# Performance work log

Hardware: AMD Instinct MI355X
Metric: run time of the kernel (lower is better)

Reference implementation:

```python
import jax, jax.numpy as jnp
from jax import lax
import numpy as np

B, N_WAY, K_SHOT, Q, IMG = 8, 5, 1, 15, 84
D = 3      # repnet spatial output for imgsz=84
CF = 64    # repnet channels
C2 = CF + 2

def _conv(x, w, b):
    y = lax.conv_general_dilated(x, w, (1, 1), 'VALID', dimension_numbers=('NCHW', 'OIHW', 'NCHW'))
    return y + b[None, :, None, None]

def _maxpool2(x):
    return lax.reduce_window(x, -jnp.inf, lax.max, (1, 1, 2, 2), (1, 1, 2, 2), 'VALID')

def _avgpool5(x):
    return lax.reduce_window(x, 0.0, lax.add, (1, 1, 5, 5), (1, 1, 5, 5), 'VALID') / 25.0

def _bn(x, g, b):
    # train-mode BatchNorm2d: batch statistics over (N, H, W), biased variance, eps=1e-5
    m = jnp.mean(x, (0, 2, 3), keepdims=True)
    v = jnp.var(x, (0, 2, 3), keepdims=True)
    return (x - m) * lax.rsqrt(v + 1e-5) * g[None, :, None, None] + b[None, :, None, None]

def _repnet(x, cw1, cb1, bg1, bb1, cw2, cb2, bg2, bb2, cw3, cb3, bg3, bb3, cw4, cb4, bg4, bb4):
    x = jax.nn.relu(_bn(_maxpool2(_conv(x, cw1, cb1)), bg1, bb1))
    x = jax.nn.relu(_bn(_maxpool2(_conv(x, cw2, cb2)), bg2, bb2))
    x = jax.nn.relu(_bn(_conv(x, cw3, cb3), bg3, bb3))
    x = jax.nn.relu(_bn(_conv(x, cw4, cb4), bg4, bb4))
    return _avgpool5(x)

def _forward(support_x, support_y, query_x, query_y, cw1, cb1, bg1, bb1, cw2, cb2, bg2, bb2, cw3, cb3, bg3, bb3, cw4, cb4, bg4, bb4, gW1, gb1, gW2, gb2, gW3, gb3, gW4, gb4, fW1, fb1, fW2, fb2, fW3, fb3, fW4, fb4):
    b, setsz = support_x.shape[:2]
    q = query_x.shape[1]
    rep = lambda z: _repnet(z, cw1, cb1, bg1, bb1, cw2, cb2, bg2, bb2, cw3, cb3, bg3, bb3, cw4, cb4, bg4, bb4)
    sup = rep(support_x.reshape(b * setsz, 3, IMG, IMG)).reshape(b, setsz, CF, D, D)
    qry = rep(query_x.reshape(b * q, 3, IMG, IMG)).reshape(b, q, CF, D, D)
    sup = sup.reshape(b, N_WAY, K_SHOT, CF, D, D).sum(2)  # sum over shots -> (b, n_way, c, d, d)
    setsz = N_WAY
    sy = support_y[:, ::K_SHOT]
    ii, jj = jnp.meshgrid(jnp.arange(D), jnp.arange(D), indexing='ij')
    coord = jnp.stack([ii, jj]).astype(jnp.float32) / D  # (2, d, d): ch0 = i/d, ch1 = j/d
    sup = jnp.concatenate([sup, jnp.broadcast_to(coord, (b, setsz, 2, D, D))], axis=2)  # (b,s,66,d,d)
    qry = jnp.concatenate([qry, jnp.broadcast_to(coord, (b, q, 2, D, D))], axis=2)      # (b,q,66,d,d)
    d2 = D * D
    sup = sup.reshape(b, setsz, C2, d2)
    qry = qry.reshape(b, q, C2, d2)
    # pair feature is cat([support_feat, query_feat]); split g's first layer so the
    # (b,q,s,d2,d2,2c) pair tensor is never materialized: g1([s;q]) = s@Ws + q@Wq + b1
    Ws, Wq = gW1[:C2], gW1[C2:]
    A = jnp.einsum('bscp,ck->bspk', sup, Ws)   # (b, s, d2, 256)
    Bq = jnp.einsum('bqcp,ck->bqpk', qry, Wq)  # (b, q, d2, 256)
    h = jax.nn.relu(A[:, None, :, :, None, :] + Bq[:, :, None, None, :, :] + gb1)  # (b,q,s,d2,d2,256)
    h = jax.nn.relu(h @ gW2 + gb2)
    h = jax.nn.relu(h @ gW3 + gb3)
    h = jax.nn.relu(h @ gW4 + gb4)
    x_f = h.sum((3, 4))  # sum over all d2*d2 pixel pairs -> (b, q, s, 256)
    h = jax.nn.relu(x_f @ fW1 + fb1)
    h = jax.nn.relu(h @ fW2 + fb2)  # nn.Dropout treated as identity (deterministic reference)
    h = jax.nn.relu(h @ fW3 + fb3)
    o = h @ fW4 + fb4  # (b, q, s, 64)
    score = jnp.sqrt(jnp.sum(o * o, axis=-1))  # L2 norm over feature dim -> (b, q, s)
    n = jnp.sqrt(jnp.sum(score * score, axis=2, keepdims=True))
    score = score / n * (n * n / (1.0 + n * n))  # squash
    ap = sy[:, None, :] == query_y[:, :, None]  # exactly one True per (b, q)
    an = ~ap
    score_ap = jnp.sum(jnp.where(ap, score, 0.0), axis=2, keepdims=True)
    MARGIN = 0.2
    loss = jnp.sum(jax.nn.relu(score - score_ap + MARGIN) * an)
    return loss

def setup_inputs() -> dict:
    key = jax.random.key(0)
    ks = iter(jax.random.split(key, 48))
    nrm = lambda shape, s: jax.random.normal(next(ks), shape, jnp.float32) * s
    inp = {}
    inp['support_x'] = nrm((B, N_WAY * K_SHOT, 3, IMG, IMG), 1.0)
    inp['support_y'] = jnp.tile(jnp.arange(N_WAY, dtype=jnp.int32), (B, 1))
    inp['query_x'] = nrm((B, Q, 3, IMG, IMG), 1.0)
    inp['query_y'] = jax.random.randint(next(ks), (B, Q), 0, N_WAY, dtype=jnp.int32)
    inp['cw1'] = nrm((64, 3, 3, 3), 0.19); inp['cb1'] = nrm((64,), 0.02)
    inp['bg1'] = 1.0 + nrm((64,), 0.05); inp['bb1'] = nrm((64,), 0.02)
    inp['cw2'] = nrm((64, 64, 3, 3), 0.042); inp['cb2'] = nrm((64,), 0.02)
    inp['bg2'] = 1.0 + nrm((64,), 0.05); inp['bb2'] = nrm((64,), 0.02)
    inp['cw3'] = nrm((64, 64, 3, 3), 0.042); inp['cb3'] = nrm((64,), 0.02)
    inp['bg3'] = 1.0 + nrm((64,), 0.05); inp['bb3'] = nrm((64,), 0.02)
    inp['cw4'] = nrm((64, 64, 3, 3), 0.042); inp['cb4'] = nrm((64,), 0.02)
    inp['bg4'] = 1.0 + nrm((64,), 0.05); inp['bb4'] = nrm((64,), 0.02)
    inp['gW1'] = nrm((2 * C2, 256), 0.087); inp['gb1'] = nrm((256,), 0.02)
    inp['gW2'] = nrm((256, 256), 0.0625); inp['gb2'] = nrm((256,), 0.02)
    inp['gW3'] = nrm((256, 256), 0.0625); inp['gb3'] = nrm((256,), 0.02)
    inp['gW4'] = nrm((256, 256), 0.0625); inp['gb4'] = nrm((256,), 0.02)
    inp['fW1'] = nrm((256, 256), 0.0625); inp['fb1'] = nrm((256,), 0.02)
    inp['fW2'] = nrm((256, 256), 0.0625); inp['fb2'] = nrm((256,), 0.02)
    inp['fW3'] = nrm((256, 128), 0.0625); inp['fb3'] = nrm((128,), 0.02)
    inp['fW4'] = nrm((128, 64), 0.088); inp['fb4'] = nrm((64,), 0.02)
    return inp

def reference(support_x, support_y, query_x, query_y, cw1, cb1, bg1, bb1, cw2, cb2, bg2, bb2, cw3, cb3, bg3, bb3, cw4, cb4, bg4, bb4, gW1, gb1, gW2, gb2, gW3, gb3, gW4, gb4, fW1, fb1, fW2, fb2, fW3, fb3, fW4, fb4):
    return _forward(support_x, support_y, query_x, query_y, cw1, cb1, bg1, bb1, cw2, cb2, bg2, bb2, cw3, cb3, bg3, bb3, cw4, cb4, bg4, bb4, gW1, gb1, gW2, gb2, gW3, gb3, gW4, gb4, fW1, fb1, fW2, fb2, fW3, fb3, fW4, fb4)
```

## Files before the change

### kernel.cpp

```cpp
#include <hip/hip_runtime.h>
#include <hip/hip_bf16.h>

typedef __hip_bfloat16 bf16;
typedef __attribute__((ext_vector_type(8))) short short8;
typedef __attribute__((ext_vector_type(4))) short bfx4;
typedef __attribute__((ext_vector_type(4))) float f32x4;

#define DEV __device__ __forceinline__

static constexpr int NSUP = 40;
static constexpr int NQRY = 120;
static constexpr int NIMG = 160;
static constexpr int GM   = 48600;
static constexpr int GMP  = 48640;
static constexpr int NBS  = 128;
static constexpr int NBQ  = 384;

DEV float b2f(short s) {
    union { unsigned int u; float f; } v; v.u = ((unsigned int)(unsigned short)s) << 16; return v.f;
}
DEV short bfbits(float v) {
    bf16 h = __float2bfloat16(v);
    union { bf16 b; short s; } u; u.b = h; return u.s;
}

DEV int xcd_swz(int b, int nwg) {
    int q = nwg >> 3, r = nwg & 7;
    int x = b & 7, i = b >> 3;
    return (x < r) ? x * (q + 1) + i : r * (q + 1) + (x - r) * q + i;
}

#define GLL(gp, lp) __builtin_amdgcn_global_load_lds( \
    (const __attribute__((address_space(1))) void*)(gp), \
    (__attribute__((address_space(3))) void*)(lp), 16, 0, 0)

__global__ void nhwc4_kernel(const float* sx, const float* qx, bf16* img) {
    int idx = blockIdx.x * 256 + threadIdx.x;
    if (idx >= NIMG * 7056) return;
    int n = idx / 7056, p = idx % 7056;
    const float* im = ((n < NSUP) ? sx + (size_t)n * 3 * 7056 : qx + (size_t)(n - NSUP) * 3 * 7056) + p;
    bfx4 o;
    o[0] = bfbits(im[0]);
    o[1] = bfbits(im[7056]);
    o[2] = bfbits(im[14112]);
    o[3] = 0;
    *(bfx4*)&img[(size_t)idx * 4] = o;
}

__global__ void prep_kernel(const float* cw1, const float* cw2, const float* cw3,
                            const float* cw4, const float* gW2, const float* gW3,
                            const float* gW4, const float* fW1, const float* fW2,
                            const float* fW3, const float* fW4, const float* fb4,
                            bf16* Wc1, bf16* Wp, bf16* WTg, bf16* fWT, float* fb4p) {
    int idx = blockIdx.x * 256 + threadIdx.x;
    if (idx < 4096) {
        int oc = idx >> 6, k = idx & 63;
        int ky = k >> 4, r = k & 15;
        float v = 0.f;
        if (ky < 3 && r < 12) {
            int kx = r >> 2, ic = r & 3;
            if (ic < 3) v = cw1[oc * 27 + ic * 9 + ky * 3 + kx];
        }
        Wc1[idx] = __float2bfloat16(v);
        return;
    }
    idx -= 4096;
    if (idx < 3 * 64 * 584) {
        int L = idx / (64 * 584), r = idx % (64 * 584);
        int oc = r / 584, kk = r % 584;
        const float* src = (L == 0) ? cw2 : (L == 1) ? cw3 : cw4;
        float v = 0.f;
        if (kk < 576) {
            int ic = kk & 63, tap = kk >> 6;
            v = src[oc * 576 + ic * 9 + tap];
        }
        Wp[idx] = __float2bfloat16(v);
        return;
    }
    idx -= 3 * 64 * 584;
    if (idx < 3 * 65536) {
        int L = idx >> 16, r = idx & 65535, n = r >> 8, k = r & 255;
        const float* W = (L == 0) ? gW2 : (L == 1) ? gW3 : gW4;
        WTg[idx] = __float2bfloat16(W[k * 256 + n]);
        return;
    }
    idx -= 3 * 65536;
    if (idx < 65536) {
        int n = idx >> 8, k = idx & 255;
        fWT[idx] = __float2bfloat16(fW1[k * 256 + n]);
    } else if (idx < 131072) {
        int r = idx - 65536, n = r >> 8, k = r & 255;
        fWT[idx] = __float2bfloat16(fW2[k * 256 + n]);
    } else if (idx < 163840) {
        int r = idx - 131072, n = r >> 8, k = r & 255;
        fWT[idx] = __float2bfloat16(fW3[k * 128 + n]);
    } else if (idx < 180224) {
        int r = idx - 163840, n = r >> 7, k = r & 127;
        float v = (n < 64) ? fW4[k * 64 + n] : 0.f;
        fWT[idx] = __float2bfloat16(v);
    } else if (idx < 180352) {
        int i = idx - 180224;
        fb4p[i] = (i < 64) ? fb4[i] : 0.f;
    }
}

__global__ __launch_bounds__(256) void conv1m_kernel(
        const bf16* __restrict__ img, const bf16* __restrict__ Wc1,
        const float* __restrict__ cb1, bf16* __restrict__ out) {
    int wid = xcd_swz(blockIdx.x, NIMG * 27);
    int n = wid / 27, chunk = wid % 27;
    int wv = threadIdx.x >> 6, ln = threadIdx.x & 63;
    int pr = ln & 15, kg = ln >> 4;
    int t0 = (chunk * 4 + wv) * 16;
    int t = t0 + pr;
    int tc = t < 1681 ? t : 1680;
    int pyt = tc / 41, pxt = tc % 41;
    const bf16* ib = img + (size_t)n * 28224;

    short8 wf[4][2];
    #pragma unroll
    for (int mt = 0; mt < 4; ++mt)
        #pragma unroll
        for (int h = 0; h < 2; ++h)
            wf[mt][h] = *(const short8*)&Wc1[(size_t)(mt * 16 + pr) * 64 + h * 32 + kg * 8];

    int r8 = (kg & 1) * 8;
    int kyb = kg >> 1;
    short8 pf[4][2];
    #pragma unroll
    for (int nt = 0; nt < 4; ++nt) {
        int py = 2 * pyt + (nt >> 1), px = 2 * pxt + (nt & 1);
        #pragma unroll
        for (int h = 0; h < 2; ++h) {
            int ky = h * 2 + kyb;
            short8 f = {0, 0, 0, 0, 0, 0, 0, 0};
            if (ky < 3) {
                const bf16* p = ib + ((py + ky) * 84 + px) * 4 + r8;
                if (r8 == 0) {
                    bfx4 a0 = *(const bfx4*)p, a1 = *(const bfx4*)(p + 4);
                    f[0] = a0[0]; f[1] = a0[1]; f[2] = a0[2]; f[3] = a0[3];
                    f[4] = a1[0]; f[5] = a1[1]; f[6] = a1[2]; f[7] = a1[3];
                } else {
                    bfx4 a0 = *(const bfx4*)p;
                    f[0] = a0[0]; f[1] = a0[1]; f[2] = a0[2]; f[3] = a0[3];
                }
            }
            pf[nt][h] = f;
        }
    }

    f32x4 acc[4][4];
    #pragma unroll
    for (int a = 0; a < 4; ++a)
        #pragma unroll
        for (int b = 0; b < 4; ++b)
            #pragma unroll
            for (int r = 0; r < 4; ++r) acc[a][b][r] = 0.f;

    #pragma unroll
    for (int h = 0; h < 2; ++h)
        #pragma unroll
        for (int mt = 0; mt < 4; ++mt)
            #pragma unroll
            for (int nt = 0; nt < 4; ++nt)
                acc[mt][nt] = __builtin_amdgcn_mfma_f32_16x16x32_bf16(
                    wf[mt][h], pf[nt][h], acc[mt][nt], 0, 0, 0);

    if (t < 1681) {
        bf16* ob = out + ((size_t)n * 1681 + t) * 64;
        #pragma unroll
        for (int mt = 0; mt < 4; ++mt) {
            f32x4 v = acc[mt][0];
            #pragma unroll
            for (int nt = 1; nt < 4; ++nt)
                #pragma unroll
                for (int r = 0; r < 4; ++r) v[r] = fmaxf(v[r], acc[mt][nt][r]);
            bfx4 o;
            #pragma unroll
            for (int r = 0; r < 4; ++r) o[r] = bfbits(v[r] + cb1[mt * 16 + kg * 4 + r]);
            *(bfx4*)&ob[mt * 16 + kg * 4] = o;
        }
    }
}

__global__ void stats_nhwc_kernel(const bf16* buf, int HW, float* partial) {
    int blk = blockIdx.x;
    bool qg = blk >= NBS;
    int b0 = qg ? blk - NBS : blk;
    int nb = qg ? NBQ : NBS;
    const bf16* base = buf + (qg ? (size_t)NSUP * HW * 64 : 0);
    long rows = (long)(qg ? NQRY : NSUP) * HW;
    int tid = threadIdx.x;
    int sub = tid & 7, rl = tid >> 3;
    float s1[8], s2[8];
    #pragma unroll
    for (int j = 0; j < 8; ++j) { s1[j] = 0.f; s2[j] = 0.f; }
    for (long r = (long)b0 * 32 + rl; r < rows; r += (long)nb * 32) {
        short8 v = *(const short8*)&base[r * 64 + sub * 8];
        #pragma unroll
        for (int j = 0; j < 8; ++j) { float f = b2f(v[j]); s1[j] += f; s2[j] += f * f; }
    }
    __shared__ float l1[256][8], l2[256][8];
    #pragma unroll
    for (int j = 0; j < 8; ++j) { l1[tid][j] = s1[j]; l2[tid][j] = s2[j]; }
    __syncthreads();
    if (tid < 64) {
        int su = tid >> 3, j = tid & 7;
        float a = 0.f, b = 0.f;
        for (int k = 0; k < 32; ++k) { a += l1[su + k * 8][j]; b += l2[su + k * 8][j]; }
        partial[blk * 128 + tid] = a;
        partial[blk * 128 + 64 + tid] = b;
    }
}

__global__ __launch_bounds__(1024) void bnfin_kernel(
        const float* partial, const float* gam, const float* bet,
        int HW, float* scsh) {
    int tid = threadIdx.x;
    int out = tid >> 3;
    int part = tid & 7;
    int g = out >> 6, c = out & 63;
    int b0 = g ? NBS : 0, nb = g ? NBQ : NBS;
    float s1 = 0.f, s2 = 0.f;
    for (int b = b0 + part; b < b0 + nb; b += 8) {
        s1 += partial[b * 128 + c];
        s2 += partial[b * 128 + 64 + c];
    }
    __shared__ float r1[1024], r2[1024];
    r1[tid] = s1; r2[tid] = s2;
    __syncthreads();
    if (part == 0) {
        #pragma unroll
        for (int j = 1; j < 8; ++j) { s1 += r1[tid + j]; s2 += r2[tid + j]; }
        float cnt = (float)((g ? NQRY : NSUP)) * (float)HW;
        float mean = s1 / cnt;
        float var = s2 / cnt - mean * mean;
        float istd = rsqrtf(var + 1e-5f);
        float sc = gam[c] * istd;
        scsh[out] = sc;
        scsh[128 + out] = bet[c] - mean * sc;
    }
}

__global__ void bnrelu_nhwc_kernel(bf16* buf, const float* scsh, int HW, int total8) {
    int idx = blockIdx.x * 256 + threadIdx.x;
    if (idx >= total8) return;
    size_t e0 = (size_t)idx * 8;
    int c0 = (int)(e0 & 63);
    int g = (int)(e0 / ((size_t)HW * 64)) >= NSUP ? 1 : 0;
    short8 v = *(short8*)&buf[e0];
    short8 o;
    #pragma unroll
    for (int j = 0; j < 8; ++j) {
        int c = c0 + j;
        float f = b2f(v[j]) * scsh[g * 64 + c] + scsh[128 + g * 64 + c];
        o[j] = bfbits(fmaxf(f, 0.f));
    }
    *(short8*)&buf[e0] = o;
}

template <int IW, int OW, bool POOL, int NT>
__global__ __launch_bounds__(256) void convmfma_kernel(
        const bf16* __restrict__ in, const bf16* __restrict__ Wp,
        const float* __restrict__ cb, bf16* __restrict__ out, int nwg) {
    constexpr int M  = OW * OW;
    constexpr int PW = OW / 2;
    constexpr int MP = POOL ? PW * PW : M;
    constexpr int T  = NIMG * MP;
    constexpr int NPF = POOL ? 4 : NT;

    int wid = xcd_swz(blockIdx.x, nwg);
    int wv = threadIdx.x >> 6, ln = threadIdx.x & 63;
    int pr = ln & 15, kg = ln >> 4;

    const bf16* pptr[NPF];
    int pxv[NPF];
    if (POOL) {
        int gp = (wid * 4 + wv) * 16 + pr;
        int gpc = gp < T ? gp : T - 1;
        pxv[0] = gp;
        int n = gpc / MP, pp = gpc % MP;
        int py = pp / PW, px = pp % PW;
        const bf16* ib = in + (size_t)n * (IW * IW * 64) + kg * 8;
        #pragma unroll
        for (int nt = 0; nt < 4; ++nt)
            pptr[nt] = ib + ((2 * py + (nt >> 1)) * IW + 2 * px + (nt & 1)) * 64;
    } else {
        #pragma unroll
        for (int nt = 0; nt < NT; ++nt) {
            int gp = (wid * 4 + wv) * (16 * NT) + nt * 16 + pr;
            int gpc = gp < T ? gp : T - 1;
            pxv[nt] = gp;
            int n = gpc / M, pix = gpc % M;
            int y = pix / OW, x = pix % OW;
            pptr[nt] = in + ((size_t)n * (IW * IW) + y * IW + x) * 64 + kg * 8;
        }
    }
    const bf16* wb = Wp + kg * 8;

    f32x4 acc[4][NPF];
    #pragma unroll
    for (int a = 0; a < 4; ++a)
        #pragma unroll
        for (int b = 0; b < NPF; ++b)
            #pragma unroll
            for (int r = 0; r < 4; ++r) acc[a][b][r] = 0.f;

    short8 pf_c[NPF];
    #pragma unroll
    for (int nt = 0; nt < NPF; ++nt) pf_c[nt] = *(const short8*)(pptr[nt]);
    #pragma unroll
    for (int s = 0; s < 18; ++s) {
        short8 pf_n[NPF];
        if (s < 17) {
            int s2 = s + 1, tap2 = s2 >> 1, h2 = s2 & 1;
            int off2 = ((tap2 / 3) * IW + (tap2 % 3)) * 64 + h2 * 32;
            #pragma unroll
            for (int nt = 0; nt < NPF; ++nt)
                pf_n[nt] = *(const short8*)(pptr[nt] + off2);
        }
        int wk = s * 32;
        short8 wf[4];
        #pragma unroll
        for (int mt = 0; mt < 4; ++mt)
            wf[mt] = *(const short8*)(wb + (size_t)(mt * 16 + pr) * 584 + wk);
        #pragma unroll
        for (int mt = 0; mt < 4; ++mt)
            #pragma unroll
            for (int nt = 0; nt < NPF; ++nt)
                acc[mt][nt] = __builtin_amdgcn_mfma_f32_16x16x32_bf16(
                    wf[mt], pf_c[nt], acc[mt][nt], 0, 0, 0);
        if (s < 17) {
            #pragma unroll
            for (int nt = 0; nt < NPF; ++nt) pf_c[nt] = pf_n[nt];
        }
    }

    if (POOL) {
        int gp = pxv[0];
        if (gp < T) {
            bf16* ob = out + (size_t)gp * 64;
            #pragma unroll
            for (int mt = 0; mt < 4; ++mt) {
                f32x4 v = acc[mt][0];
                #pragma unroll
                for (int nt = 1; nt < 4; ++nt)
                    #pragma unroll
                    for (int r = 0; r < 4; ++r) v[r] = fmaxf(v[r], acc[mt][nt][r]);
                bfx4 o;
                #pragma unroll
                for (int r = 0; r < 4; ++r) o[r] = bfbits(v[r] + cb[mt * 16 + kg * 4 + r]);
                *(bfx4*)&ob[mt * 16 + kg * 4] = o;
            }
        }
    } else {
        #pragma unroll
        for (int mt = 0; mt < 4; ++mt) {
            float bv[4];
            #pragma unroll
            for (int r = 0; r < 4; ++r) bv[r] = cb[mt * 16 + kg * 4 + r];
            #pragma unroll
            for (int nt = 0; nt < NPF; ++nt) {
                if (pxv[nt] < T) {
                    bfx4 o;
                    #pragma unroll
                    for (int r = 0; r < 4; ++r) o[r] = bfbits(acc[mt][nt][r] + bv[r]);
                    *(bfx4*)&out[(size_t)pxv[nt] * 64 + mt * 16 + kg * 4] = o;
                }
            }
        }
    }
}

__global__ void bnpool_kernel(const bf16* buf4, const float* scsh, float* feat) {
    int wid = blockIdx.x * 4 + (threadIdx.x >> 6);
    int c = threadIdx.x & 63;
    if (wid >= 1440) return;
    int n = wid / 9, p9 = wid % 9;
    int g = n >= NSUP;
    float sc = scsh[g * 64 + c], sh = scsh[128 + g * 64 + c];
    int ii = p9 / 3, jj = p9 % 3;
    const bf16* base = buf4 + ((size_t)n * 225 + ii * 5 * 15 + jj * 5) * 64 + c;
    float s = 0;
    #pragma unroll
    for (int u = 0; u < 5; ++u)
        #pragma unroll
        for (int v = 0; v < 5; ++v)
            s += fmaxf(__bfloat162float(base[(u * 15 + v) * 64]) * sc + sh, 0.f);
    feat[n * 576 + c * 9 + p9] = s * 0.04f;
}

__global__ void proj_kernel(const float* feat, const float* gW1, float* A, float* Bq) {
    int n = blockIdx.x, k = threadIdx.x;
    const float* W = (n < NSUP) ? gW1 : gW1 + 66 * 256;
    float* out = (n < NSUP) ? A + (size_t)n * 9 * 256 : Bq + (size_t)(n - NSUP) * 9 * 256;
    const float* fb = feat + n * 576;
    for (int p = 0; p < 9; ++p) {
        float acc = 0;
        for (int c = 0; c < 64; ++c) acc += fb[c * 9 + p] * W[c * 256 + k];
        acc += ((float)(p / 3) * (1.f / 3.f)) * W[64 * 256 + k];
        acc += ((float)(p % 3) * (1.f / 3.f)) * W[65 * 256 + k];
        out[p * 256 + k] = acc;
    }
}

__global__ __launch_bounds__(512) void gmlp_fused_kernel(
        const float* __restrict__ A, const float* __restrict__ Bq,
        const float* __restrict__ gb1, const bf16* __restrict__ WTg,
        const float* __restrict__ gb2, const float* __restrict__ gb3,
        const float* __restrict__ gb4, bf16* __restrict__ H3) {
    __shared__ __align__(16) short hs[128 * 256];
    int tid = threadIdx.x;
    int r0 = blockIdx.x * 128;

    #pragma unroll
    for (int i = 0; i < 8; ++i) {
        int row = (tid >> 5) + i * 16;
        int c8 = tid & 31;
        int col = c8 * 8;
        int grow = r0 + row;
        short8 o = {0, 0, 0, 0, 0, 0, 0, 0};
        if (grow < GM) {
            int bqs = grow / 81, r81 = grow % 81;
            int ps = r81 / 9, pq = r81 % 9;
            int b = bqs / 75, r75 = bqs % 75, q = r75 / 5, s5 = r75 % 5;
            const float* Ar = A + ((size_t)((b * 5 + s5) * 9 + ps)) * 256 + col;
            const float* Br = Bq + ((size_t)((b * 15 + q) * 9 + pq)) * 256 + col;
            #pragma unroll
            for (int j = 0; j < 8; ++j)
                o[j] = bfbits(fmaxf(Ar[j] + Br[j] + gb1[col + j], 0.f));
        }
        int c8s = c8 ^ (row & 7);
        *(short8*)&hs[row * 256 + c8s * 8] = o;
    }
    __syncthreads();

    int wv = tid >> 6, ln = tid & 63;
    int wr = wv >> 2, wc = wv & 3;
    int pr = ln & 15, kg = ln >> 4;

    #pragma unroll
    for (int L = 0; L < 3; ++L) {
        const bf16* WT = WTg + L * 65536;
        const float* bias = (L == 0) ? gb2 : (L == 1) ? gb3 : gb4;

        f32x4 acc[4][4];
        #pragma unroll
        for (int n = 0; n < 4; ++n)
            #pragma unroll
            for (int m = 0; m < 4; ++m)
                #pragma unroll
                for (int r = 0; r < 4; ++r) acc[n][m][r] = 0.f;

        #pragma unroll
        for (int kt = 0; kt < 8; ++kt) {
            short8 a[4], b[4];
            #pragma unroll
            for (int m = 0; m < 4; ++m) {
                int row = wr * 64 + m * 16 + pr;
                int c8 = kt * 4 + kg;
                int c8s = c8 ^ (row & 7);
                a[m] = *(const short8*)&hs[row * 256 + c8s * 8];
            }
            #pragma unroll
            for (int n = 0; n < 4; ++n)
                b[n] = *(const short8*)&WT[(size_t)(wc * 64 + n * 16 + pr) * 256 + kt * 32 + kg * 8];
            #pragma unroll
            for (int n = 0; n < 4; ++n)
                #pragma unroll
                for (int m = 0; m < 4; ++m)
                    acc[n][m] = __builtin_amdgcn_mfma_f32_16x16x32_bf16(b[n], a[m], acc[n][m], 0, 0, 0);
        }

        __syncthreads();
        #pragma unroll
        for (int n = 0; n < 4; ++n) {
            int ch = wc * 64 + n * 16 + kg * 4;
            f32x4 bv = *(const f32x4*)&bias[ch];
            #pragma unroll
            for (int m = 0; m < 4; ++m) {
                int hrow = wr * 64 + m * 16 + pr;
                bfx4 o;
                #pragma unroll
                for (int r = 0; r < 4; ++r)
                    o[r] = bfbits(fmaxf(acc[n][m][r] + bv[r], 0.f));
                if (L < 2) {
                    int c8s = (ch >> 3) ^ (hrow & 7);
                    *(bfx4*)&hs[hrow * 256 + c8s * 8 + (ch & 7)] = o;
                } else {
                    *(bfx4*)&H3[(size_t)(r0 + hrow) * 256 + ch] = o;
                }
            }
        }
        if (L < 2) __syncthreads();
    }
}

template <int KT, bool RELU, bool F32OUT>
__global__ __launch_bounds__(256) void gemm_f_kernel(
        const bf16* __restrict__ Ain, const bf16* __restrict__ WT,
        const float* __restrict__ bias, void* __restrict__ outv, int ldo) {
    constexpr int K = KT * 32;
    __shared__ __align__(16) short As[2][4096];
    __shared__ __align__(16) short Bs[2][4096];
    int bm0 = blockIdx.x * 128;
    int bn0 = blockIdx.y * 128;
    int tid = threadIdx.x, wv = tid >> 6, ln = tid & 63;
    int wm = wv >> 1, wn = wv & 1;

    int srow = (wv * 2) * 16 + (ln >> 2);
    int scol = (ln & 3) * 8;
    const bf16* Ag = Ain + (size_t)(bm0 + srow) * K + scol;
    const bf16* Bg = WT + (size_t)(bn0 + srow) * K + scol;

    f32x4 acc[4][4];
    #pragma unroll
    for (int m = 0; m < 4; ++m)
        #pragma unroll
        for (int n = 0; n < 4; ++n)
            #pragma unroll
            for (int r = 0; r < 4; ++r) acc[m][n][r] = 0.f;

    int ar = (wm * 64 + (ln & 15)) * 32 + (ln >> 4) * 8;
    int br = (wn * 64 + (ln & 15)) * 32 + (ln >> 4) * 8;

    GLL(Ag,          &As[0][(wv * 2) * 512]);
    GLL(Ag + 16 * K, &As[0][(wv * 2 + 1) * 512]);
    GLL(Bg,          &Bs[0][(wv * 2) * 512]);
    GLL(Bg + 16 * K, &Bs[0][(wv * 2 + 1) * 512]);
    __syncthreads();

    int cur = 0;
    for (int kt = 0; kt < KT; ++kt) {
        if (kt < KT - 1) {
            int k0 = (kt + 1) * 32;
            GLL(Ag + k0,          &As[cur ^ 1][(wv * 2) * 512]);
            GLL(Ag + 16 * K + k0, &As[cur ^ 1][(wv * 2 + 1) * 512]);
            GLL(Bg + k0,          &Bs[cur ^ 1][(wv * 2) * 512]);
            GLL(Bg + 16 * K + k0, &Bs[cur ^ 1][(wv * 2 + 1) * 512]);
        }
        short8 a[4], b[4];
        #pragma unroll
        for (int m = 0; m < 4; ++m) a[m] = *(const short8*)&As[cur][ar + m * 512];
        #pragma unroll
        for (int n = 0; n < 4; ++n) b[n] = *(const short8*)&Bs[cur][br + n * 512];
        #pragma unroll
        for (int m = 0; m < 4; ++m)
            #pragma unroll
            for (int n = 0; n < 4; ++n)
                acc[m][n] = __builtin_amdgcn_mfma_f32_16x16x32_bf16(a[m], b[n], acc[m][n], 0, 0, 0);
        __syncthreads();
        cur ^= 1;
    }

    int orow = bm0 + wm * 64 + (ln >> 4) * 4;
    int ocol = bn0 + wn * 64 + (ln & 15);
    #pragma unroll
    for (int n = 0; n < 4; ++n) {
        float bv = bias[ocol + n * 16];
        #pragma unroll
        for (int m = 0; m < 4; ++m) {
            #pragma unroll
            for (int r = 0; r < 4; ++r) {
                float v = acc[m][n][r] + bv;
                if (RELU) v = fmaxf(v, 0.f);
                size_t oi = (size_t)(orow + m * 16 + r) * ldo + ocol + n * 16;
                if (F32OUT) ((float*)outv)[oi] = v;
                else        ((bf16*)outv)[oi] = __float2bfloat16(v);
            }
        }
    }
}

__global__ void xfred_kernel(const bf16* H, bf16* xfb) {
    int bqs = blockIdx.x, tid = threadIdx.x;
    int sub = tid & 31, rl = tid >> 5;
    float s[8];
    #pragma unroll
    for (int j = 0; j < 8; ++j) s[j] = 0.f;
    if (bqs < 600) {
        const bf16* p = H + (size_t)bqs * 81 * 256 + sub * 8;
        for (int r = rl; r < 81; r += 8) {
            short8 v = *(const short8*)&p[r * 256];
            #pragma unroll
            for (int j = 0; j < 8; ++j) s[j] += b2f(v[j]);
        }
    }
    __shared__ float red[256][8];
    #pragma unroll
    for (int j = 0; j < 8; ++j) red[tid][j] = s[j];
    __syncthreads();
    if (tid < 32) {
        short8 o;
        #pragma unroll
        for (int j = 0; j < 8; ++j) {
            float t = 0;
            #pragma unroll
            for (int k = 0; k < 8; ++k) t += red[k * 32 + tid][j];
            o[j] = bfbits(t);
        }
        *(short8*)&xfb[(size_t)bqs * 256 + tid * 8] = o;
    }
}

__global__ void score_kernel(const float* F4, const int* sy, const int* qy, float* lossp) {
    __shared__ float scs[8];
    int bid = blockIdx.x;
    int tid = threadIdx.x;
    int s = tid >> 6, k = tid & 63;
    float v = F4[(size_t)(bid * 5 + s) * 128 + k];
    float sum = v * v;
    #pragma unroll
    for (int m = 1; m < 64; m <<= 1) sum += __shfl_xor(sum, m);
    if (k == 0) scs[s] = sqrtf(sum);
    __syncthreads();
    if (tid == 0) {
        int b = bid / 15, q = bid % 15;
        float n2 = 0;
        for (int j = 0; j < 5; ++j) n2 += scs[j] * scs[j];
        float n = sqrtf(n2);
        float f = n / (1.f + n2);
        int qyv = qy[b * 15 + q];
        float sc[5]; bool ap[5]; float sap = 0;
        for (int j = 0; j < 5; ++j) {
            sc[j] = scs[j] * f;
            ap[j] = (sy[b * 5 + j] == qyv);
            if (ap[j]) sap += sc[j];
        }
        float lp = 0;
        for (int j = 0; j < 5; ++j)
            if (!ap[j]) lp += fmaxf(sc[j] - sap + 0.2f, 0.f);
        lossp[bid] = lp;
    }
}

__global__ void lreduce_kernel(const float* lossp, float* out) {
    __shared__ float r[128];
    int tid = threadIdx.x;
    r[tid] = (tid < NQRY) ? lossp[tid] : 0.f;
    __syncthreads();
    for (int off = 64; off; off >>= 1) {
        if (tid < off) r[tid] += r[tid + off];
        __syncthreads();
    }
    if (tid == 0) out[0] = r[0];
}

extern "C" void kernel_launch(void* const* d_in, const int* in_sizes, int n_in,
                              void* d_out, int out_size, void* d_ws, size_t ws_size,
                              hipStream_t stream) {
    const float* sx  = (const float*)d_in[0];
    const int*   syp = (const int*)d_in[1];
    const float* qx  = (const float*)d_in[2];
    const int*   qyp = (const int*)d_in[3];
    const float* cw1 = (const float*)d_in[4];  const float* cb1 = (const float*)d_in[5];
    const float* bg1 = (const float*)d_in[6];  const float* bb1 = (const float*)d_in[7];
    const float* cw2 = (const float*)d_in[8];  const float* cb2 = (const float*)d_in[9];
    const float* bg2 = (const float*)d_in[10]; const float* bb2 = (const float*)d_in[11];
    const float* cw3 = (const float*)d_in[12]; const float* cb3 = (const float*)d_in[13];
    const float* bg3 = (const float*)d_in[14]; const float* bb3 = (const float*)d_in[15];
    const float* cw4 = (const float*)d_in[16]; const float* cb4 = (const float*)d_in[17];
    const float* bg4 = (const float*)d_in[18]; const float* bb4 = (const float*)d_in[19];
    const float* gW1 = (const float*)d_in[20]; const float* gb1 = (const float*)d_in[21];
    const float* gW2 = (const float*)d_in[22]; const float* gb2 = (const float*)d_in[23];
    const float* gW3 = (const float*)d_in[24]; const float* gb3 = (const float*)d_in[25];
    const float* gW4 = (const float*)d_in[26]; const float* gb4 = (const float*)d_in[27];
    const float* fW1 = (const float*)d_in[28]; const float* fb1 = (const float*)d_in[29];
    const float* fW2 = (const float*)d_in[30]; const float* fb2 = (const float*)d_in[31];
    const float* fW3 = (const float*)d_in[32]; const float* fb3 = (const float*)d_in[33];
    const float* fW4 = (const float*)d_in[34]; const float* fb4 = (const float*)d_in[35];

    char* w = (char*)d_ws;
    size_t off = 0;
    bf16*  buf1  = (bf16*)(w + off); off += 34426880ull;
    bf16*  H3    = (bf16*)(w + off); off += 31150080ull;
    bf16*  pbuf2 = (bf16*)(w + off); off += 7393280ull;
    bf16*  buf3  = (bf16*)(w + off); off += 5918720ull;
    bf16*  buf4  = (bf16*)(w + off); off += 4608000ull;
    float* feat  = (float*)(w + off); off += 368640ull;
    float* Abuf  = (float*)(w + off); off += 368640ull;
    float* Bbuf  = (float*)(w + off); off += 1105920ull;
    bf16*  xfb   = (bf16*)(w + off); off += 327680ull;
    bf16*  F1    = (bf16*)(w + off); off += 327680ull;
    bf16*  F2    = (bf16*)(w + off); off += 327680ull;
    bf16*  F3    = (bf16*)(w + off); off += 163840ull;
    float* F4    = (float*)(w + off); off += 327680ull;
    float* partial = (float*)(w + off); off += 262144ull;
    float* scsh  = (float*)(w + off); off += 4096ull;
    bf16*  imgN  = (bf16*)(w + off); off += 9031680ull;
    bf16*  Wc1   = (bf16*)(w + off); off += 8192ull;
    bf16*  Wp    = (bf16*)(w + off); off += 224256ull;
    bf16*  WTg   = (bf16*)(w + off); off += 393216ull;
    bf16*  fWT   = (bf16*)(w + off); off += 360448ull;
    float* fb4p  = (float*)(w + off); off += 512ull;
    float* lossp = (float*)(w + off); off += 512ull;

    float* scsh1 = scsh;        float* scsh2 = scsh + 256;
    float* scsh3 = scsh + 512;  float* scsh4 = scsh + 768;
    bf16* Wp2 = Wp;
    bf16* Wp3 = Wp + 64 * 584;
    bf16* Wp4 = Wp + 2 * 64 * 584;
    bf16* fWT1 = fWT;
    bf16* fWT2 = fWT + 65536;
    bf16* fWT3 = fWT + 131072;
    bf16* fWT4 = fWT + 163840;

    nhwc4_kernel<<<(NIMG * 7056 + 255) / 256, 256, 0, stream>>>(sx, qx, imgN);
    prep_kernel<<<(493184 + 255) / 256, 256, 0, stream>>>(
        cw1, cw2, cw3, cw4, gW2, gW3, gW4, fW1, fW2, fW3, fW4, fb4,
        Wc1, Wp, WTg, fWT, fb4p);

    conv1m_kernel<<<NIMG * 27, 256, 0, stream>>>(imgN, Wc1, cb1, buf1);
    stats_nhwc_kernel<<<NBS + NBQ, 256, 0, stream>>>(buf1, 1681, partial);
    bnfin_kernel<<<1, 1024, 0, stream>>>(partial, bg1, bb1, 1681, scsh1);
    bnrelu_nhwc_kernel<<<(2151680 + 255) / 256, 256, 0, stream>>>(buf1, scsh1, 1681, 2151680);

    convmfma_kernel<41, 39, true, 4><<<dim3(903), 256, 0, stream>>>(buf1, Wp2, cb2, pbuf2, 903);
    stats_nhwc_kernel<<<NBS + NBQ, 256, 0, stream>>>(pbuf2, 361, partial);
    bnfin_kernel<<<1, 1024, 0, stream>>>(partial, bg2, bb2, 361, scsh2);
    bnrelu_nhwc_kernel<<<(462080 + 255) / 256, 256, 0, stream>>>(pbuf2, scsh2, 361, 462080);

    convmfma_kernel<19, 17, false, 2><<<dim3(362), 256, 0, stream>>>(pbuf2, Wp3, cb3, buf3, 362);
    stats_nhwc_kernel<<<NBS + NBQ, 256, 0, stream>>>(buf3, 289, partial);
    bnfin_kernel<<<1, 1024, 0, stream>>>(partial, bg3, bb3, 289, scsh3);
    bnrelu_nhwc_kernel<<<(369920 + 255) / 256, 256, 0, stream>>>(buf3, scsh3, 289, 369920);

    convmfma_kernel<17, 15, false, 2><<<dim3(282), 256, 0, stream>>>(buf3, Wp4, cb4, buf4, 282);
    stats_nhwc_kernel<<<NBS + NBQ, 256, 0, stream>>>(buf4, 225, partial);
    bnfin_kernel<<<1, 1024, 0, stream>>>(partial, bg4, bb4, 225, scsh4);
    bnpool_kernel<<<360, 256, 0, stream>>>(buf4, scsh4, feat);

    proj_kernel<<<NIMG, 256, 0, stream>>>(feat, gW1, Abuf, Bbuf);

    gmlp_fused_kernel<<<GMP / 128, 512, 0, stream>>>(Abuf, Bbuf, gb1, WTg, gb2, gb3, gb4, H3);
    xfred_kernel<<<640, 256, 0, stream>>>(H3, xfb);

    gemm_f_kernel<8, true,  false><<<dim3(5, 2), 256, 0, stream>>>(xfb, fWT1, fb1,  (void*)F1, 256);
    gemm_f_kernel<8, true,  false><<<dim3(5, 2), 256, 0, stream>>>(F1,  fWT2, fb2,  (void*)F2, 256);
    gemm_f_kernel<8, true,  false><<<dim3(5, 1), 256, 0, stream>>>(F2,  fWT3, fb3,  (void*)F3, 128);
    gemm_f_kernel<4, false, true ><<<dim3(5, 1), 256, 0, stream>>>(F3,  fWT4, fb4p, (void*)F4, 128);

    score_kernel<<<NQRY, 320, 0, stream>>>(F4, syp, qyp, lossp);
    lreduce_kernel<<<1, 128, 0, stream>>>(lossp, (float*)d_out);
}
```

Measured before the change: 367.2 us.

## Unfuse g-MLP into separate h0 build and three tiled GEMM launches

Result: faster. 358.3 us (-2.4%).

```diff
diff --git a/kernel.cpp b/kernel.cpp
--- a/kernel.cpp
+++ b/kernel.cpp
@@ -404,96 +404,27 @@
     }
 }
 
-__global__ __launch_bounds__(512) void gmlp_fused_kernel(
-        const float* __restrict__ A, const float* __restrict__ Bq,
-        const float* __restrict__ gb1, const bf16* __restrict__ WTg,
-        const float* __restrict__ gb2, const float* __restrict__ gb3,
-        const float* __restrict__ gb4, bf16* __restrict__ H3) {
-    __shared__ __align__(16) short hs[128 * 256];
+__global__ void h0_kernel(const float* A, const float* Bq, const float* gb1, bf16* H) {
     int tid = threadIdx.x;
-    int r0 = blockIdx.x * 128;
-
-    #pragma unroll
-    for (int i = 0; i < 8; ++i) {
-        int row = (tid >> 5) + i * 16;
-        int c8 = tid & 31;
-        int col = c8 * 8;
-        int grow = r0 + row;
-        short8 o = {0, 0, 0, 0, 0, 0, 0, 0};
-        if (grow < GM) {
-            int bqs = grow / 81, r81 = grow % 81;
-            int ps = r81 / 9, pq = r81 % 9;
-            int b = bqs / 75, r75 = bqs % 75, q = r75 / 5, s5 = r75 % 5;
-            const float* Ar = A + ((size_t)((b * 5 + s5) * 9 + ps)) * 256 + col;
-            const float* Br = Bq + ((size_t)((b * 15 + q) * 9 + pq)) * 256 + col;
-            #pragma unroll
-            for (int j = 0; j < 8; ++j)
-                o[j] = bfbits(fmaxf(Ar[j] + Br[j] + gb1[col + j], 0.f));
-        }
-        int c8s = c8 ^ (row & 7);
-        *(short8*)&hs[row * 256 + c8s * 8] = o;
-    }
-    __syncthreads();
-
-    int wv = tid >> 6, ln = tid & 63;
-    int wr = wv >> 2, wc = wv & 3;
-    int pr = ln & 15, kg = ln >> 4;
-
-    #pragma unroll
-    for (int L = 0; L < 3; ++L) {
-        const bf16* WT = WTg + L * 65536;
-        const float* bias = (L == 0) ? gb2 : (L == 1) ? gb3 : gb4;
-
-        f32x4 acc[4][4];
-        #pragma unroll
-        for (int n = 0; n < 4; ++n)
-            #pragma unroll
-            for (int m = 0; m < 4; ++m)
-                #pragma unroll
-                for (int r = 0; r < 4; ++r) acc[n][m][r] = 0.f;
-
-        #pragma unroll
-        for (int kt = 0; kt < 8; ++kt) {
-            short8 a[4], b[4];
-            #pragma unroll
-            for (int m = 0; m < 4; ++m) {
-                int row = wr * 64 + m * 16 + pr;
-                int c8 = kt * 4 + kg;
-                int c8s = c8 ^ (row & 7);
-                a[m] = *(const short8*)&hs[row * 256 + c8s * 8];
-            }
-            #pragma unroll
-            for (int n = 0; n < 4; ++n)
-                b[n] = *(const short8*)&WT[(size_t)(wc * 64 + n * 16 + pr) * 256 + kt * 32 + kg * 8];
-            #pragma unroll
-            for (int n = 0; n < 4; ++n)
-                #pragma unroll
-                for (int m = 0; m < 4; ++m)
-                    acc[n][m] = __builtin_amdgcn_mfma_f32_16x16x32_bf16(b[n], a[m], acc[n][m], 0, 0, 0);
-        }
-
-        __syncthreads();
-        #pragma unroll
-        for (int n = 0; n < 4; ++n) {
-            int ch = wc * 64 + n * 16 + kg * 4;
-            f32x4 bv = *(const f32x4*)&bias[ch];
-            #pragma unroll
-            for (int m = 0; m < 4; ++m) {
-                int hrow = wr * 64 + m * 16 + pr;
-                bfx4 o;
-                #pragma unroll
-                for (int r = 0; r < 4; ++r)
-                    o[r] = bfbits(fmaxf(acc[n][m][r] + bv[r], 0.f));
-                if (L < 2) {
-                    int c8s = (ch >> 3) ^ (hrow & 7);
-                    *(bfx4*)&hs[hrow * 256 + c8s * 8 + (ch & 7)] = o;
-                } else {
-                    *(bfx4*)&H3[(size_t)(r0 + hrow) * 256 + ch] = o;
-                }
-            }
-        }
-        if (L < 2) __syncthreads();
-    }
+    int row = blockIdx.x * 8 + (tid >> 5);
+    int col = (tid & 31) * 8;
+    short8 o;
+    if (row < GM) {
+        int bqs = row / 81, r81 = row % 81;
+        int ps = r81 / 9, pq = r81 % 9;
+        int b = bqs / 75, r75 = bqs % 75, q = r75 / 5, s = r75 % 5;
+        const float* Ar = A + ((size_t)((b * 5 + s) * 9 + ps)) * 256 + col;
+        const float* Br = Bq + ((size_t)((b * 15 + q) * 9 + pq)) * 256 + col;
+        #pragma unroll
+        for (int j = 0; j < 8; ++j) {
+            float v = Ar[j] + Br[j] + gb1[col + j];
+            o[j] = bfbits(fmaxf(v, 0.f));
+        }
+    } else {
+        #pragma unroll
+        for (int j = 0; j < 8; ++j) o[j] = 0;
+    }
+    *(short8*)&H[(size_t)row * 256 + col] = o;
 }
 
 template <int KT, bool RELU, bool F32OUT>
@@ -673,7 +604,7 @@
     char* w = (char*)d_ws;
     size_t off = 0;
     bf16*  buf1  = (bf16*)(w + off); off += 34426880ull;
-    bf16*  H3    = (bf16*)(w + off); off += 31150080ull;
+    bf16*  hbuf  = (bf16*)(w + off); off += 31150080ull;
     bf16*  pbuf2 = (bf16*)(w + off); off += 7393280ull;
     bf16*  buf3  = (bf16*)(w + off); off += 5918720ull;
     bf16*  buf4  = (bf16*)(w + off); off += 4608000ull;
@@ -705,6 +636,9 @@
     bf16* fWT3 = fWT + 131072;
     bf16* fWT4 = fWT + 163840;
 
+    bf16* Hb0 = buf1;
+    bf16* Hb1 = hbuf;
+
     nhwc4_kernel<<<(NIMG * 7056 + 255) / 256, 256, 0, stream>>>(sx, qx, imgN);
     prep_kernel<<<(493184 + 255) / 256, 256, 0, stream>>>(
         cw1, cw2, cw3, cw4, gW2, gW3, gW4, fW1, fW2, fW3, fW4, fb4,
@@ -732,8 +666,12 @@
 
     proj_kernel<<<NIMG, 256, 0, stream>>>(feat, gW1, Abuf, Bbuf);
 
-    gmlp_fused_kernel<<<GMP / 128, 512, 0, stream>>>(Abuf, Bbuf, gb1, WTg, gb2, gb3, gb4, H3);
-    xfred_kernel<<<640, 256, 0, stream>>>(H3, xfb);
+    h0_kernel<<<GMP / 8, 256, 0, stream>>>(Abuf, Bbuf, gb1, Hb0);
+    dim3 ggrid(GMP / 128, 2);
+    gemm_f_kernel<8, true, false><<<ggrid, 256, 0, stream>>>(Hb0, WTg,          gb2, (void*)Hb1, 256);
+    gemm_f_kernel<8, true, false><<<ggrid, 256, 0, stream>>>(Hb1, WTg + 65536,  gb3, (void*)Hb0, 256);
+    gemm_f_kernel<8, true, false><<<ggrid, 256, 0, stream>>>(Hb0, WTg + 131072, gb4, (void*)Hb1, 256);
+    xfred_kernel<<<640, 256, 0, stream>>>(Hb1, xfb);
 
     gemm_f_kernel<8, true,  false><<<dim3(5, 2), 256, 0, stream>>>(xfb, fWT1, fb1,  (void*)F1, 256);
     gemm_f_kernel<8, true,  false><<<dim3(5, 2), 256, 0, stream>>>(F1,  fWT2, fb2,  (void*)F2, 256);
```
